# Kernel optimization log

Hardware: AMD Instinct MI355X
Metric: run time of the kernel (lower is better)

## Reference

```python
import jax, jax.numpy as jnp
import numpy as np

N = 30000  # nodes per type (drug and protein)


def graph_conv(x, s, d, W, b):
    # DGL GraphConv, norm='both': h = D_in^{-1/2} A (D_out^{-1/2} x) W + b
    ones = jnp.ones(s.shape, dtype=x.dtype)
    deg_out = jnp.maximum(jax.ops.segment_sum(ones, s, num_segments=N), 1.0)
    deg_in = jnp.maximum(jax.ops.segment_sum(ones, d, num_segments=N), 1.0)
    xh = (x * deg_out[:, None] ** -0.5) @ W          # transform first (in > out)
    agg = jax.ops.segment_sum(xh[s], d, num_segments=N)  # gather-scatter over edges
    return agg * deg_in[:, None] ** -0.5 + b


def rgcn_channel(xd, xp, src_c, dst_c, W1c, b1c, W2c, b2c):
    # relations: 0 drug->drug, 1 drug->protein, 2 protein->drug, 3 protein->protein
    hd = jax.nn.relu(graph_conv(xd, src_c[0], dst_c[0], W1c[0], b1c[0])
                     + graph_conv(xp, src_c[2], dst_c[2], W1c[2], b1c[2]))
    hp = jax.nn.relu(graph_conv(xd, src_c[1], dst_c[1], W1c[1], b1c[1])
                     + graph_conv(xp, src_c[3], dst_c[3], W1c[3], b1c[3]))
    hd2 = jax.nn.relu(graph_conv(hd, src_c[0], dst_c[0], W2c[0], b2c[0])
                      + graph_conv(hp, src_c[2], dst_c[2], W2c[2], b2c[2]))
    hp2 = jax.nn.relu(graph_conv(hd, src_c[1], dst_c[1], W2c[1], b2c[1])
                      + graph_conv(hp, src_c[3], dst_c[3], W2c[3], b2c[3]))
    return hd2, hp2


def semantic_attention(z, Wp, bp, q):
    # z: [N, K, F] -> beta [K], emb [N, F]
    w = jnp.tanh(z @ Wp + bp) @ q            # [N, K]
    beta = jax.nn.softmax(jnp.mean(w, axis=0))  # [K]
    return beta, jnp.einsum('k,nkf->nf', beta, z)


def setup_inputs() -> dict:
    key = jax.random.key(0)
    ks = jax.random.split(key, 8)
    E = 250000
    in_f, hid_f, out_f = 512, 256, 128
    x_drug = jax.random.normal(ks[0], (N, in_f), dtype=jnp.float32)
    x_pro = jax.random.normal(ks[1], (N, in_f), dtype=jnp.float32)
    src = jax.random.randint(ks[2], (4, 4, E), 0, N, dtype=jnp.int32)
    dst = jax.random.randint(ks[3], (4, 4, E), 0, N, dtype=jnp.int32)
    W1 = jax.random.normal(ks[4], (4, 4, in_f, hid_f), dtype=jnp.float32) / np.sqrt(in_f)
    b1 = jnp.zeros((4, 4, hid_f), dtype=jnp.float32)
    W2 = jax.random.normal(ks[5], (4, 4, hid_f, out_f), dtype=jnp.float32) / np.sqrt(hid_f)
    b2 = jnp.zeros((4, 4, out_f), dtype=jnp.float32)
    Wp = jax.random.normal(ks[6], (out_f, out_f), dtype=jnp.float32) / np.sqrt(out_f)
    bp = jnp.zeros((out_f,), dtype=jnp.float32)
    q = jax.random.normal(ks[7], (out_f,), dtype=jnp.float32) / np.sqrt(out_f)
    return {"x_drug": x_drug, "x_pro": x_pro, "src": src, "dst": dst,
            "W1": W1, "b1": b1, "W2": W2, "b2": b2, "Wp": Wp, "bp": bp, "q": q}


def reference(x_drug, x_pro, src, dst, W1, b1, W2, b2, Wp, bp, q):
    h_drug, h_pro = [], []
    for c in range(4):  # 4 channel graphs (fixed small loop)
        hd, hp = rgcn_channel(x_drug, x_pro, src[c], dst[c], W1[c], b1[c], W2[c], b2[c])
        h_drug.append(hd)
        h_pro.append(hp)
    # MCKRL stacks channels 0, 2, 3 only
    z_drug = jnp.stack([h_drug[0], h_drug[2], h_drug[3]], axis=1)  # [N,3,F]
    z_pro = jnp.stack([h_pro[0], h_pro[2], h_pro[3]], axis=1)
    beta_drug, emb_drug = semantic_attention(z_drug, Wp, bp, q)
    beta_pro, emb_pro = semantic_attention(z_pro, Wp, bp, q)
    return emb_drug, emb_pro, beta_drug, beta_pro
```

## Files before the change

### kernel.cpp

```cpp
#include <hip/hip_runtime.h>
#include <math.h>


#define IN_F  512
#define HID_F 256
#define OUT_F 128
#define NG    12
#define NPART 16
#define RANGE 1875
#define ES    8

typedef _Float16 f16x2 __attribute__((ext_vector_type(2)));
typedef _Float16 f16x4 __attribute__((ext_vector_type(4)));
typedef _Float16 f16x8 __attribute__((ext_vector_type(8)));
typedef float    f32x4 __attribute__((ext_vector_type(4)));

#define AS1 __attribute__((address_space(1)))
#define AS3 __attribute__((address_space(3)))

__device__ __forceinline__ void gld16(const void* g, void* l) {
    __builtin_amdgcn_global_load_lds((const AS1 void*)g, (AS3 void*)l, 16, 0, 0);
}

__host__ __device__ __forceinline__ int chan_of(int ci) { return ci == 0 ? 0 : ci + 1; }

__global__ __launch_bounds__(512) void k_hist(const int* __restrict__ src,
                                              const int* __restrict__ dst,
                                              int* __restrict__ hin,
                                              int* __restrict__ hout,
                                              int N, int E) {
    __shared__ int hi[RANGE], ho[RANGE];
    int g = blockIdx.x, p = blockIdx.y, es = blockIdx.z, t = threadIdx.x;
    for (int i = t; i < RANGE; i += 512) { hi[i] = 0; ho[i] = 0; }
    __syncthreads();
    int ci = g >> 2, c = chan_of(ci), r = g & 3;
    const int* sp = src + (size_t)(c * 4 + r) * E;
    const int* dp = dst + (size_t)(c * 4 + r) * E;
    int lo = p * RANGE;
    int sl = E / ES;
    int e0 = es * sl, e1 = (es == ES - 1) ? E : e0 + sl;
    for (int e = e0 + t; e < e1; e += 512) {
        int s = sp[e] - lo;
        int d = dp[e] - lo;
        if ((unsigned)s < (unsigned)RANGE) atomicAdd(&ho[s], 1);
        if ((unsigned)d < (unsigned)RANGE) atomicAdd(&hi[d], 1);
    }
    __syncthreads();
    int* hing  = hin  + ((size_t)g * ES + es) * N;
    int* houtg = hout + ((size_t)g * ES + es) * N;
    for (int i = t; i < RANGE; i += 512) {
        int node = lo + i;
        if (node < N) { hing[node] = hi[i]; houtg[node] = ho[i]; }
    }
}

__global__ void k_rs2(const int* __restrict__ hin, const int* __restrict__ hout,
                      int* __restrict__ deg_in,
                      float* __restrict__ rs_out, float* __restrict__ rs_in, int N) {
    int i = blockIdx.x * 256 + threadIdx.x;
    if (i >= NG * N) return;
    int g = i / N, n = i - g * N;
    int di = 0, dq = 0;
#pragma unroll
    for (int es = 0; es < ES; ++es) {
        di += hin [((size_t)g * ES + es) * N + n];
        dq += hout[((size_t)g * ES + es) * N + n];
    }
    deg_in[i] = di;
    rs_in[i]  = rsqrtf(fmaxf((float)di, 1.0f));
    rs_out[i] = rsqrtf(fmaxf((float)dq, 1.0f));
}

__global__ __launch_bounds__(1024) void k_scan(const int* __restrict__ deg_in,
                                               int* __restrict__ row_ptr, int N) {
    int g = blockIdx.x;
    const int* dg = deg_in + (size_t)g * N;
    int* rp = row_ptr + (size_t)g * (N + 1);
    __shared__ int wsum[16];
    int tid = threadIdx.x;
    int lane = tid & 63, wv = tid >> 6;
    int run = 0;
    for (int basei = 0; basei < N; basei += 1024) {
        int i = basei + tid;
        int v = (i < N) ? dg[i] : 0;
        int x = v;
#pragma unroll
        for (int off = 1; off < 64; off <<= 1) {
            int y = __shfl_up(x, off);
            if (lane >= off) x += y;
        }
        if (lane == 63) wsum[wv] = x;
        __syncthreads();
        if (wv == 0) {
            int s = (lane < 16) ? wsum[lane] : 0;
#pragma unroll
            for (int off = 1; off < 16; off <<= 1) {
                int y = __shfl_up(s, off);
                if (lane >= off) s += y;
            }
            if (lane < 16) wsum[lane] = s;
        }
        __syncthreads();
        int woff = wv ? wsum[wv - 1] : 0;
        if (i < N) rp[i] = run + woff + x - v;
        run += wsum[15];
        __syncthreads();
    }
    if (tid == 0) rp[N] = run;
}

__global__ __launch_bounds__(512) void k_fill3(const int* __restrict__ src,
                                               const int* __restrict__ dst,
                                               const int* __restrict__ row_ptr,
                                               const int* __restrict__ hin,
                                               int* __restrict__ col, int N, int E) {
    __shared__ int cur[RANGE];
    int g = blockIdx.x, p = blockIdx.y, es = blockIdx.z, t = threadIdx.x;
    int lo = p * RANGE;
    const int* rp = row_ptr + (size_t)g * (N + 1);
    for (int i = t; i < RANGE; i += 512) {
        int node = lo + i;
        int base = 0;
        if (node < N) {
            base = rp[node];
            for (int e2 = 0; e2 < es; ++e2)
                base += hin[((size_t)g * ES + e2) * N + node];
        }
        cur[i] = base;
    }
    __syncthreads();
    int ci = g >> 2, c = chan_of(ci), r = g & 3;
    const int* sp = src + (size_t)(c * 4 + r) * E;
    const int* dp = dst + (size_t)(c * 4 + r) * E;
    int* cg = col + (size_t)g * E;
    int sl = E / ES;
    int e0 = es * sl, e1 = (es == ES - 1) ? E : e0 + sl;
    for (int e = e0 + t; e < e1; e += 512) {
        int s = sp[e];
        int d = dp[e] - lo;
        if ((unsigned)d < (unsigned)RANGE) {
            int pos = atomicAdd(&cur[d], 1);
            cg[pos] = s;
        }
    }
}

__global__ void k_cvt16(const float* __restrict__ in, _Float16* __restrict__ out,
                        size_t n) {
    size_t i = ((size_t)blockIdx.x * 256 + threadIdx.x) * 8;
    if (i >= n) return;
    float4 a = *(const float4*)(in + i);
    float4 b = *(const float4*)(in + i + 4);
    f16x8 v;
    v[0] = (_Float16)a.x; v[1] = (_Float16)a.y; v[2] = (_Float16)a.z; v[3] = (_Float16)a.w;
    v[4] = (_Float16)b.x; v[5] = (_Float16)b.y; v[6] = (_Float16)b.z; v[7] = (_Float16)b.w;
    *(f16x8*)(out + i) = v;
}

__global__ __launch_bounds__(256) void k_cvtT(const float* __restrict__ W,
                                              _Float16* __restrict__ out,
                                              int K, int Nn) {
    __shared__ float tile[32][33];
    int gi = blockIdx.z, ci = gi >> 2, c = chan_of(ci), r = gi & 3;
    const float* Wg = W + (size_t)(c * 4 + r) * K * Nn;
    _Float16* Wo = out + ((size_t)(ci * 2 + (r >> 1)) * 2 * Nn + (size_t)(r & 1) * Nn) * K;
    int k0 = blockIdx.x * 32, n0 = blockIdx.y * 32;
    int tx = threadIdx.x & 31, ty = threadIdx.x >> 5;
    for (int yy = ty; yy < 32; yy += 8)
        tile[yy][tx] = Wg[(size_t)(k0 + yy) * Nn + n0 + tx];
    __syncthreads();
    for (int yy = ty; yy < 32; yy += 8)
        Wo[(size_t)(n0 + yy) * K + k0 + tx] = (_Float16)tile[tx][yy];
}

__global__ __launch_bounds__(256) void k_cvtWp(const float* __restrict__ Wp,
                                               _Float16* __restrict__ WpT) {
    __shared__ float tile[32][33];
    int k0 = blockIdx.x * 32, n0 = blockIdx.y * 32;
    int tx = threadIdx.x & 31, ty = threadIdx.x >> 5;
    for (int yy = ty; yy < 32; yy += 8)
        tile[yy][tx] = Wp[(size_t)(k0 + yy) * 128 + n0 + tx];
    __syncthreads();
    for (int yy = ty; yy < 32; yy += 8)
        WpT[(size_t)(n0 + yy) * 128 + k0 + tx] = (_Float16)tile[tx][yy];
}

__global__ __launch_bounds__(256) void k_gemm16(const _Float16* __restrict__ A0, size_t Azs,
                                                const _Float16* __restrict__ B0, size_t Bzs,
                                                _Float16* __restrict__ C0, size_t Czs,
                                                const float* __restrict__ rs0, int rsN,
                                                int Nsplit,
                                                int M, int K, int Nn) {
    const _Float16* A = A0 + (size_t)blockIdx.z * Azs;
    const _Float16* Bt = B0 + (size_t)blockIdx.z * Bzs;
    _Float16* C = C0 + (size_t)blockIdx.z * Czs;
    const float* rsA = rs0 ? rs0 + (size_t)(2 * blockIdx.z) * rsN : nullptr;
    __shared__ __align__(16) _Float16 As[128 * 64];
    __shared__ __align__(16) _Float16 Bs[128 * 64];
    int t = threadIdx.x;
    int lane = t & 63, wid = t >> 6;
    int wm = wid >> 1, wn = wid & 1;
    int brow = blockIdx.y * 128, bcol = blockIdx.x * 128;

    f32x4 acc[4][4] = {};
    int mrow = lane & 15;
    int khalf = lane >> 4;

    for (int k0 = 0; k0 < K; k0 += 64) {
        __syncthreads();
#pragma unroll
        for (int i = 0; i < 4; ++i) {
            int L = t + i * 256;
            int row = L >> 3, spp = L & 7;
            int sg = spp ^ (row & 7);
            int ra = brow + row; if (ra > M - 1) ra = M - 1;
            gld16((const void*)(A + (size_t)ra * K + (size_t)(k0 + sg * 8)),
                  (void*)(As + (size_t)(i * 256 + wid * 64) * 8));
            int rb = bcol + row;
            gld16((const void*)(Bt + (size_t)rb * K + (size_t)(k0 + sg * 8)),
                  (void*)(Bs + (size_t)(i * 256 + wid * 64) * 8));
        }
        __syncthreads();
#pragma unroll
        for (int ks = 0; ks < 2; ++ks) {
            f16x8 af[4], bf[4];
#pragma unroll
            for (int mi = 0; mi < 4; ++mi) {
                int r = wm * 64 + mi * 16 + mrow;
                int s = ks * 4 + khalf;
                int ph = s ^ (r & 7);
                af[mi] = *(const f16x8*)(As + r * 64 + ph * 8);
            }
#pragma unroll
            for (int ni = 0; ni < 4; ++ni) {
                int r = wn * 64 + ni * 16 + mrow;
                int s = ks * 4 + khalf;
                int ph = s ^ (r & 7);
                bf[ni] = *(const f16x8*)(Bs + r * 64 + ph * 8);
            }
#pragma unroll
            for (int mi = 0; mi < 4; ++mi)
#pragma unroll
                for (int ni = 0; ni < 4; ++ni)
                    acc[mi][ni] = __builtin_amdgcn_mfma_f32_16x16x32_f16(
                        af[mi], bf[ni], acc[mi][ni], 0, 0, 0);
        }
    }
#pragma unroll
    for (int mi = 0; mi < 4; ++mi) {
#pragma unroll
        for (int r = 0; r < 4; ++r) {
            int row = brow + wm * 64 + mi * 16 + (lane >> 4) * 4 + r;
            if (row < M) {
                float sA = 1.0f, sB = 1.0f;
                if (rsA) { sA = rsA[row]; sB = rsA[rsN + row]; }
#pragma unroll
                for (int ni = 0; ni < 4; ++ni) {
                    int colx = bcol + wn * 64 + ni * 16 + (lane & 15);
                    float sc = (colx < Nsplit) ? sA : sB;
                    C[(size_t)row * Nn + colx] = (_Float16)(acc[mi][ni][r] * sc);
                }
            }
        }
    }
}

template<typename FV, int VEC>
__device__ __forceinline__ void agg_body(const _Float16* __restrict__ Ya0,
                                         const _Float16* __restrict__ Yb0, int ystride,
                                         const int* __restrict__ row_ptr,
                                         const int* __restrict__ col,
                                         const float* __restrict__ rs_in,
                                         int ga0, int gb0,
                                         const float* __restrict__ ba0,
                                         const float* __restrict__ bb0,
                                         _Float16* __restrict__ outb,
                                         size_t out_sidestride, int ostride,
                                         int F, int N, int E) {
    int wv = threadIdx.x >> 6, lane = threadIdx.x & 63;
    int i = blockIdx.x * 4 + wv;
    if (i >= N) return;
    int side = blockIdx.y;
    int f0 = VEC * lane;
    const _Float16* Ya = Ya0 + side * F;
    const _Float16* Yb = Yb0 + side * F;
    int ga = ga0 + side, gb = gb0 + side;

    float accA[VEC] = {}, accB[VEC] = {};
    {
        const int* rp = row_ptr + (size_t)ga * (N + 1);
        const int* cg = col + (size_t)ga * E;
        int beg = rp[i], end = rp[i + 1];
        for (int e = beg; e < end; e += 4) {
            int s0 = cg[e];
            bool b1 = e + 1 < end, b2 = e + 2 < end, b3 = e + 3 < end;
            int s1 = b1 ? cg[e + 1] : s0;
            int s2 = b2 ? cg[e + 2] : s0;
            int s3 = b3 ? cg[e + 3] : s0;
            FV v0 = *(const FV*)(Ya + (size_t)s0 * ystride + f0);
            FV v1 = *(const FV*)(Ya + (size_t)s1 * ystride + f0);
            FV v2 = *(const FV*)(Ya + (size_t)s2 * ystride + f0);
            FV v3 = *(const FV*)(Ya + (size_t)s3 * ystride + f0);
            float m1 = b1 ? 1.0f : 0.0f, m2 = b2 ? 1.0f : 0.0f, m3 = b3 ? 1.0f : 0.0f;
#pragma unroll
            for (int k = 0; k < VEC; ++k)
                accA[k] += (float)v0[k] + m1 * (float)v1[k]
                         + m2 * (float)v2[k] + m3 * (float)v3[k];
        }
    }
    {
        const int* rp = row_ptr + (size_t)gb * (N + 1);
        const int* cg = col + (size_t)gb * E;
        int beg = rp[i], end = rp[i + 1];
        for (int e = beg; e < end; e += 4) {
            int s0 = cg[e];
            bool b1 = e + 1 < end, b2 = e + 2 < end, b3 = e + 3 < end;
            int s1 = b1 ? cg[e + 1] : s0;
            int s2 = b2 ? cg[e + 2] : s0;
            int s3 = b3 ? cg[e + 3] : s0;
            FV v0 = *(const FV*)(Yb + (size_t)s0 * ystride + f0);
            FV v1 = *(const FV*)(Yb + (size_t)s1 * ystride + f0);
            FV v2 = *(const FV*)(Yb + (size_t)s2 * ystride + f0);
            FV v3 = *(const FV*)(Yb + (size_t)s3 * ystride + f0);
            float m1 = b1 ? 1.0f : 0.0f, m2 = b2 ? 1.0f : 0.0f, m3 = b3 ? 1.0f : 0.0f;
#pragma unroll
            for (int k = 0; k < VEC; ++k)
                accB[k] += (float)v0[k] + m1 * (float)v1[k]
                         + m2 * (float)v2[k] + m3 * (float)v3[k];
        }
    }
    float ria = rs_in[(size_t)ga * N + i];
    float rib = rs_in[(size_t)gb * N + i];
    FV o;
#pragma unroll
    for (int k = 0; k < VEC; ++k) {
        float v = ria * accA[k] + rib * accB[k]
                + ba0[side * F + f0 + k] + bb0[side * F + f0 + k];
        o[k] = (_Float16)fmaxf(v, 0.0f);
    }
    *(FV*)(outb + side * out_sidestride + (size_t)i * ostride + f0) = o;
}

__global__ __launch_bounds__(256) void k_agg256(const _Float16* Ya0, const _Float16* Yb0,
                                                int ystride, const int* row_ptr, const int* col,
                                                const float* rs_in, int ga0, int gb0,
                                                const float* ba0, const float* bb0,
                                                _Float16* outb, size_t oss, int ostride,
                                                int N, int E) {
    agg_body<f16x4, 4>(Ya0, Yb0, ystride, row_ptr, col, rs_in, ga0, gb0,
                       ba0, bb0, outb, oss, ostride, 256, N, E);
}

__global__ __launch_bounds__(256) void k_agg128(const _Float16* Ya0, const _Float16* Yb0,
                                                int ystride, const int* row_ptr, const int* col,
                                                const float* rs_in, int ga0, int gb0,
                                                const float* ba0, const float* bb0,
                                                _Float16* outb, size_t oss, int ostride,
                                                int N, int E) {
    agg_body<f16x2, 2>(Ya0, Yb0, ystride, row_ptr, col, rs_in, ga0, gb0,
                       ba0, bb0, outb, oss, ostride, 128, N, E);
}

__global__ __launch_bounds__(256) void k_wred(const _Float16* __restrict__ T,
                                              const float* __restrict__ bp,
                                              const float* __restrict__ q,
                                              float* __restrict__ w_all, int N) {
    int m = blockIdx.x * 4 + (threadIdx.x >> 6);
    int lane = threadIdx.x & 63;
    if (m >= 6 * N) return;
    f16x2 v2 = *(const f16x2*)(T + (size_t)m * 128 + 2 * lane);
    float v = tanhf((float)v2[0] + bp[2 * lane]) * q[2 * lane]
            + tanhf((float)v2[1] + bp[2 * lane + 1]) * q[2 * lane + 1];
#pragma unroll
    for (int o = 1; o < 64; o <<= 1) v += __shfl_xor(v, o);
    if (lane == 0) {
        int side = m / (3 * N);
        int rem = m - side * 3 * N;
        int node = rem / 3, k = rem - node * 3;
        w_all[((size_t)side * 3 + k) * N + node] = v;
    }
}

__global__ __launch_bounds__(256) void k_beta(const float* __restrict__ w_all,
                                              float* __restrict__ beta_ws,
                                              float* __restrict__ beta_out, int N) {
    int side = blockIdx.x;
    int tid = threadIdx.x;
    __shared__ float red[256];
    float sums[3];
    for (int k = 0; k < 3; ++k) {
        float s = 0.0f;
        for (int i = tid; i < N; i += 256) s += w_all[((size_t)side * 3 + k) * N + i];
        red[tid] = s;
        __syncthreads();
        for (int off = 128; off > 0; off >>= 1) {
            if (tid < off) red[tid] += red[tid + off];
            __syncthreads();
        }
        sums[k] = red[0];
        __syncthreads();
    }
    if (tid == 0) {
        float inv = 1.0f / (float)N;
        float m0 = sums[0] * inv, m1 = sums[1] * inv, m2 = sums[2] * inv;
        float mx = fmaxf(m0, fmaxf(m1, m2));
        float e0 = expf(m0 - mx), e1 = expf(m1 - mx), e2 = expf(m2 - mx);
        float denom = e0 + e1 + e2;
        float b0 = e0 / denom, b1 = e1 / denom, b2 = e2 / denom;
        beta_ws[side * 3 + 0] = b0; beta_out[side * 3 + 0] = b0;
        beta_ws[side * 3 + 1] = b1; beta_out[side * 3 + 1] = b1;
        beta_ws[side * 3 + 2] = b2; beta_out[side * 3 + 2] = b2;
    }
}

__global__ __launch_bounds__(64) void k_emb(const _Float16* __restrict__ z,
                                            const float* __restrict__ beta_ws,
                                            float* __restrict__ out, int N) {
    int i = blockIdx.x, side = blockIdx.y, t = threadIdx.x;
    const _Float16* zr = z + (size_t)side * N * 384 + (size_t)i * 384;
    const float* b = beta_ws + side * 3;
    f16x2 z0 = *(const f16x2*)(zr + 2 * t);
    f16x2 z1 = *(const f16x2*)(zr + 128 + 2 * t);
    f16x2 z2 = *(const f16x2*)(zr + 256 + 2 * t);
    float2 o;
    o.x = b[0] * (float)z0[0] + b[1] * (float)z1[0] + b[2] * (float)z2[0];
    o.y = b[0] * (float)z0[1] + b[1] * (float)z1[1] + b[2] * (float)z2[1];
    *(float2*)&out[(size_t)side * N * 128 + (size_t)i * 128 + 2 * t] = o;
}

extern "C" void kernel_launch(void* const* d_in, const int* in_sizes, int n_in,
                              void* d_out, int out_size, void* d_ws, size_t ws_size,
                              hipStream_t stream) {
    const float* x_drug = (const float*)d_in[0];
    const float* x_pro  = (const float*)d_in[1];
    const int*   src    = (const int*)d_in[2];
    const int*   dst    = (const int*)d_in[3];
    const float* W1     = (const float*)d_in[4];
    const float* b1     = (const float*)d_in[5];
    const float* W2     = (const float*)d_in[6];
    const float* b2     = (const float*)d_in[7];
    const float* Wp     = (const float*)d_in[8];
    const float* bp     = (const float*)d_in[9];
    const float* q      = (const float*)d_in[10];
    float* out = (float*)d_out;

    const int N = in_sizes[0] / IN_F;
    const int E = in_sizes[2] / 16;

    size_t off = 0;
    auto alloc = [&](size_t bytes) -> void* {
        void* p = (char*)d_ws + off;
        off += (bytes + 255) & ~(size_t)255;
        return p;
    };
    int*      deg_in  = (int*)alloc((size_t)NG * N * 4);
    int*      row_ptr = (int*)alloc((size_t)NG * (N + 1) * 4);
    int*      col     = (int*)alloc((size_t)NG * E * 4);
    float*    rs_out  = (float*)alloc((size_t)NG * N * 4);
    float*    rs_in   = (float*)alloc((size_t)NG * N * 4);
    _Float16* xh      = (_Float16*)alloc((size_t)2 * N * IN_F * 2);
    _Float16* W1cat   = (_Float16*)alloc((size_t)6 * 2 * HID_F * IN_F * 2);
    _Float16* W2cat   = (_Float16*)alloc((size_t)6 * 2 * OUT_F * HID_F * 2);
    _Float16* WpT     = (_Float16*)alloc((size_t)128 * 128 * 2);
    _Float16* Y1      = (_Float16*)alloc((size_t)2 * N * 512 * 2);
    _Float16* Y2      = (_Float16*)alloc((size_t)2 * N * 256 * 2);
    _Float16* H1      = (_Float16*)alloc((size_t)2 * N * HID_F * 2);
    _Float16* zbuf    = (_Float16*)alloc((size_t)2 * N * 384 * 2);
    float*    w_all   = (float*)alloc((size_t)2 * 3 * N * 4);
    float*    beta_ws = (float*)alloc(64);
    int*      hin  = (int*)Y1;
    int*      hout = hin + (size_t)NG * ES * N;
    _Float16* T    = Y1;
    (void)ws_size; (void)n_in; (void)out_size;

    dim3 hg(NG, NPART, ES);
    k_hist<<<hg, 512, 0, stream>>>(src, dst, hin, hout, N, E);
    k_rs2<<<(NG * N + 255) / 256, 256, 0, stream>>>(hin, hout, deg_in, rs_out, rs_in, N);
    k_scan<<<NG, 1024, 0, stream>>>(deg_in, row_ptr, N);
    k_fill3<<<hg, 512, 0, stream>>>(src, dst, row_ptr, hin, col, N, E);

    size_t nx = (size_t)N * IN_F;
    k_cvt16<<<(int)((nx / 8 + 255) / 256), 256, 0, stream>>>(x_drug, xh, nx);
    k_cvt16<<<(int)((nx / 8 + 255) / 256), 256, 0, stream>>>(x_pro,  xh + nx, nx);
    k_cvtT<<<dim3(IN_F / 32, HID_F / 32, NG), 256, 0, stream>>>(W1, W1cat, IN_F, HID_F);
    k_cvtT<<<dim3(HID_F / 32, OUT_F / 32, NG), 256, 0, stream>>>(W2, W2cat, HID_F, OUT_F);
    k_cvtWp<<<dim3(4, 4), 256, 0, stream>>>(Wp, WpT);

    dim3 g1(512 / 128, (N + 127) / 128, 2);
    dim3 g2(256 / 128, (N + 127) / 128, 2);
    dim3 agrid((N + 3) / 4, 2);
    dim3 egrid(N, 2);

    for (int ci = 0; ci < 3; ++ci) {
        int c = chan_of(ci);
        k_gemm16<<<g1, 256, 0, stream>>>(xh, (size_t)N * IN_F,
                                         W1cat + (size_t)ci * 2 * 512 * 512, (size_t)512 * 512,
                                         Y1, (size_t)N * 512,
                                         rs_out + (size_t)ci * 4 * N, N, 256,
                                         N, IN_F, 512);
        k_agg256<<<agrid, 256, 0, stream>>>(Y1, Y1 + (size_t)N * 512, 512,
                                            row_ptr, col, rs_in,
                                            ci * 4 + 0, ci * 4 + 2,
                                            b1 + (size_t)c * 4 * HID_F, b1 + (size_t)(c * 4 + 2) * HID_F,
                                            H1, (size_t)N * HID_F, HID_F, N, E);
        k_gemm16<<<g2, 256, 0, stream>>>(H1, (size_t)N * HID_F,
                                         W2cat + (size_t)ci * 2 * 256 * 256, (size_t)256 * 256,
                                         Y2, (size_t)N * 256,
                                         rs_out + (size_t)ci * 4 * N, N, 128,
                                         N, HID_F, 256);
        k_agg128<<<agrid, 256, 0, stream>>>(Y2, Y2 + (size_t)N * 256, 256,
                                            row_ptr, col, rs_in,
                                            ci * 4 + 0, ci * 4 + 2,
                                            b2 + (size_t)c * 4 * OUT_F, b2 + (size_t)(c * 4 + 2) * OUT_F,
                                            zbuf + (size_t)ci * OUT_F, (size_t)N * 384, 384, N, E);
    }

    int Mrows = 2 * N * 3;
    dim3 gT(1, (Mrows + 127) / 128, 1);
    k_gemm16<<<gT, 256, 0, stream>>>(zbuf, 0, WpT, 0, T, 0,
                                     nullptr, 0, 0, Mrows, 128, 128);
    k_wred<<<(Mrows + 3) / 4, 256, 0, stream>>>(T, bp, q, w_all, N);
    k_beta<<<2, 256, 0, stream>>>(w_all, beta_ws, out + (size_t)2 * N * OUT_F, N);
    k_emb<<<egrid, 64, 0, stream>>>(zbuf, beta_ws, out, N);
}
```

Measured before the change: 1.216 ms.

## Unroll aggregation gather by 8, parallelize beta reduction, batch emb and convert launches

The aggregation kernel's two relation loops become one unrolled loop that gathers eight neighbor rows per iteration instead of four, which raises memory-level parallelism for the irregular gathers. The semantic-attention beta reduction is split into a wide partial-sum kernel and a small finalize kernel, replacing the two-block serial reduction. The embedding kernel now packs four rows per 256-thread block instead of one row per 64-thread block. The two fp16 input conversions are merged into one launch. The wider unroll raises register pressure and adds masked work on short adjacency lists.

```diff
diff --git a/kernel.cpp b/kernel.cpp
--- a/kernel.cpp
+++ b/kernel.cpp
@@ -9,6 +9,7 @@
 #define NPART 16
 #define RANGE 1875
 #define ES    8
+#define BCH   32
 
 typedef _Float16 f16x2 __attribute__((ext_vector_type(2)));
 typedef _Float16 f16x4 __attribute__((ext_vector_type(4)));
@@ -145,16 +146,17 @@
     }
 }
 
-__global__ void k_cvt16(const float* __restrict__ in, _Float16* __restrict__ out,
-                        size_t n) {
+__global__ void k_cvt16b(const float* __restrict__ inA, const float* __restrict__ inB,
+                         _Float16* __restrict__ out, size_t n) {
     size_t i = ((size_t)blockIdx.x * 256 + threadIdx.x) * 8;
     if (i >= n) return;
+    const float* in = blockIdx.y ? inB : inA;
     float4 a = *(const float4*)(in + i);
     float4 b = *(const float4*)(in + i + 4);
     f16x8 v;
     v[0] = (_Float16)a.x; v[1] = (_Float16)a.y; v[2] = (_Float16)a.z; v[3] = (_Float16)a.w;
     v[4] = (_Float16)b.x; v[5] = (_Float16)b.y; v[6] = (_Float16)b.z; v[7] = (_Float16)b.w;
-    *(f16x8*)(out + i) = v;
+    *(f16x8*)(out + blockIdx.y * n + i) = v;
 }
 
 __global__ __launch_bounds__(256) void k_cvtT(const float* __restrict__ W,
@@ -282,59 +284,41 @@
     if (i >= N) return;
     int side = blockIdx.y;
     int f0 = VEC * lane;
-    const _Float16* Ya = Ya0 + side * F;
-    const _Float16* Yb = Yb0 + side * F;
-    int ga = ga0 + side, gb = gb0 + side;
-
-    float accA[VEC] = {}, accB[VEC] = {};
-    {
-        const int* rp = row_ptr + (size_t)ga * (N + 1);
-        const int* cg = col + (size_t)ga * E;
+    const _Float16* Ybase[2] = { Ya0 + side * F, Yb0 + side * F };
+    int gg[2] = { ga0 + side, gb0 + side };
+
+    float accT[2][VEC] = {};
+#pragma unroll
+    for (int h = 0; h < 2; ++h) {
+        const int* rp = row_ptr + (size_t)gg[h] * (N + 1);
+        const int* cg = col + (size_t)gg[h] * E;
+        const _Float16* Y = Ybase[h];
         int beg = rp[i], end = rp[i + 1];
-        for (int e = beg; e < end; e += 4) {
-            int s0 = cg[e];
-            bool b1 = e + 1 < end, b2 = e + 2 < end, b3 = e + 3 < end;
-            int s1 = b1 ? cg[e + 1] : s0;
-            int s2 = b2 ? cg[e + 2] : s0;
-            int s3 = b3 ? cg[e + 3] : s0;
-            FV v0 = *(const FV*)(Ya + (size_t)s0 * ystride + f0);
-            FV v1 = *(const FV*)(Ya + (size_t)s1 * ystride + f0);
-            FV v2 = *(const FV*)(Ya + (size_t)s2 * ystride + f0);
-            FV v3 = *(const FV*)(Ya + (size_t)s3 * ystride + f0);
-            float m1 = b1 ? 1.0f : 0.0f, m2 = b2 ? 1.0f : 0.0f, m3 = b3 ? 1.0f : 0.0f;
-#pragma unroll
-            for (int k = 0; k < VEC; ++k)
-                accA[k] += (float)v0[k] + m1 * (float)v1[k]
-                         + m2 * (float)v2[k] + m3 * (float)v3[k];
-        }
-    }
-    {
-        const int* rp = row_ptr + (size_t)gb * (N + 1);
-        const int* cg = col + (size_t)gb * E;
-        int beg = rp[i], end = rp[i + 1];
-        for (int e = beg; e < end; e += 4) {
-            int s0 = cg[e];
-            bool b1 = e + 1 < end, b2 = e + 2 < end, b3 = e + 3 < end;
-            int s1 = b1 ? cg[e + 1] : s0;
-            int s2 = b2 ? cg[e + 2] : s0;
-            int s3 = b3 ? cg[e + 3] : s0;
-            FV v0 = *(const FV*)(Yb + (size_t)s0 * ystride + f0);
-            FV v1 = *(const FV*)(Yb + (size_t)s1 * ystride + f0);
-            FV v2 = *(const FV*)(Yb + (size_t)s2 * ystride + f0);
-            FV v3 = *(const FV*)(Yb + (size_t)s3 * ystride + f0);
-            float m1 = b1 ? 1.0f : 0.0f, m2 = b2 ? 1.0f : 0.0f, m3 = b3 ? 1.0f : 0.0f;
-#pragma unroll
-            for (int k = 0; k < VEC; ++k)
-                accB[k] += (float)v0[k] + m1 * (float)v1[k]
-                         + m2 * (float)v2[k] + m3 * (float)v3[k];
-        }
-    }
-    float ria = rs_in[(size_t)ga * N + i];
-    float rib = rs_in[(size_t)gb * N + i];
+        for (int e = beg; e < end; e += 8) {
+            int idx[8]; float m[8]; FV v[8];
+            idx[0] = cg[e]; m[0] = 1.0f;
+#pragma unroll
+            for (int u = 1; u < 8; ++u) {
+                bool ok = (e + u < end);
+                idx[u] = ok ? cg[e + u] : idx[0];
+                m[u] = ok ? 1.0f : 0.0f;
+            }
+#pragma unroll
+            for (int u = 0; u < 8; ++u)
+                v[u] = *(const FV*)(Y + (size_t)idx[u] * ystride + f0);
+#pragma unroll
+            for (int u = 0; u < 8; ++u)
+#pragma unroll
+                for (int k = 0; k < VEC; ++k)
+                    accT[h][k] = fmaf(m[u], (float)v[u][k], accT[h][k]);
+        }
+    }
+    float ria = rs_in[(size_t)gg[0] * N + i];
+    float rib = rs_in[(size_t)gg[1] * N + i];
     FV o;
 #pragma unroll
     for (int k = 0; k < VEC; ++k) {
-        float v = ria * accA[k] + rib * accB[k]
+        float v = ria * accT[0][k] + rib * accT[1][k]
                 + ba0[side * F + f0 + k] + bb0[side * F + f0 + k];
         o[k] = (_Float16)fmaxf(v, 0.0f);
     }
@@ -381,28 +365,43 @@
     }
 }
 
-__global__ __launch_bounds__(256) void k_beta(const float* __restrict__ w_all,
+__global__ __launch_bounds__(256) void k_beta1(const float* __restrict__ w_all,
+                                               float* __restrict__ partials, int N) {
+    int chunk = blockIdx.x, k = blockIdx.y, side = blockIdx.z;
+    const float* w = w_all + ((size_t)side * 3 + k) * N;
+    int per = (N + BCH - 1) / BCH;
+    int i0 = chunk * per;
+    int i1 = i0 + per; if (i1 > N) i1 = N;
+    int tid = threadIdx.x;
+    float s = 0.0f;
+    for (int i = i0 + tid; i < i1; i += 256) s += w[i];
+    __shared__ float red[256];
+    red[tid] = s;
+    __syncthreads();
+    for (int off = 128; off > 0; off >>= 1) {
+        if (tid < off) red[tid] += red[tid + off];
+        __syncthreads();
+    }
+    if (tid == 0) partials[((size_t)side * 3 + k) * BCH + chunk] = red[0];
+}
+
+__global__ __launch_bounds__(64) void k_beta2(const float* __restrict__ partials,
                                               float* __restrict__ beta_ws,
                                               float* __restrict__ beta_out, int N) {
-    int side = blockIdx.x;
+    __shared__ float sums[6];
     int tid = threadIdx.x;
-    __shared__ float red[256];
-    float sums[3];
-    for (int k = 0; k < 3; ++k) {
+    if (tid < 6) {
         float s = 0.0f;
-        for (int i = tid; i < N; i += 256) s += w_all[((size_t)side * 3 + k) * N + i];
-        red[tid] = s;
-        __syncthreads();
-        for (int off = 128; off > 0; off >>= 1) {
-            if (tid < off) red[tid] += red[tid + off];
-            __syncthreads();
-        }
-        sums[k] = red[0];
-        __syncthreads();
-    }
-    if (tid == 0) {
+        for (int j = 0; j < BCH; ++j) s += partials[(size_t)tid * BCH + j];
+        sums[tid] = s;
+    }
+    __syncthreads();
+    if (tid < 2) {
+        int side = tid;
         float inv = 1.0f / (float)N;
-        float m0 = sums[0] * inv, m1 = sums[1] * inv, m2 = sums[2] * inv;
+        float m0 = sums[side * 3 + 0] * inv;
+        float m1 = sums[side * 3 + 1] * inv;
+        float m2 = sums[side * 3 + 2] * inv;
         float mx = fmaxf(m0, fmaxf(m1, m2));
         float e0 = expf(m0 - mx), e1 = expf(m1 - mx), e2 = expf(m2 - mx);
         float denom = e0 + e1 + e2;
@@ -413,10 +412,12 @@
     }
 }
 
-__global__ __launch_bounds__(64) void k_emb(const _Float16* __restrict__ z,
-                                            const float* __restrict__ beta_ws,
-                                            float* __restrict__ out, int N) {
-    int i = blockIdx.x, side = blockIdx.y, t = threadIdx.x;
+__global__ __launch_bounds__(256) void k_emb(const _Float16* __restrict__ z,
+                                             const float* __restrict__ beta_ws,
+                                             float* __restrict__ out, int N) {
+    int i = blockIdx.x * 4 + (threadIdx.x >> 6);
+    if (i >= N) return;
+    int side = blockIdx.y, t = threadIdx.x & 63;
     const _Float16* zr = z + (size_t)side * N * 384 + (size_t)i * 384;
     const float* b = beta_ws + side * 3;
     f16x2 z0 = *(const f16x2*)(zr + 2 * t);
@@ -467,6 +468,7 @@
     _Float16* H1      = (_Float16*)alloc((size_t)2 * N * HID_F * 2);
     _Float16* zbuf    = (_Float16*)alloc((size_t)2 * N * 384 * 2);
     float*    w_all   = (float*)alloc((size_t)2 * 3 * N * 4);
+    float*    partials= (float*)alloc((size_t)6 * BCH * 4);
     float*    beta_ws = (float*)alloc(64);
     int*      hin  = (int*)Y1;
     int*      hout = hin + (size_t)NG * ES * N;
@@ -480,8 +482,7 @@
     k_fill3<<<hg, 512, 0, stream>>>(src, dst, row_ptr, hin, col, N, E);
 
     size_t nx = (size_t)N * IN_F;
-    k_cvt16<<<(int)((nx / 8 + 255) / 256), 256, 0, stream>>>(x_drug, xh, nx);
-    k_cvt16<<<(int)((nx / 8 + 255) / 256), 256, 0, stream>>>(x_pro,  xh + nx, nx);
+    k_cvt16b<<<dim3((int)((nx / 8 + 255) / 256), 2), 256, 0, stream>>>(x_drug, x_pro, xh, nx);
     k_cvtT<<<dim3(IN_F / 32, HID_F / 32, NG), 256, 0, stream>>>(W1, W1cat, IN_F, HID_F);
     k_cvtT<<<dim3(HID_F / 32, OUT_F / 32, NG), 256, 0, stream>>>(W2, W2cat, HID_F, OUT_F);
     k_cvtWp<<<dim3(4, 4), 256, 0, stream>>>(Wp, WpT);
@@ -489,7 +490,6 @@
     dim3 g1(512 / 128, (N + 127) / 128, 2);
     dim3 g2(256 / 128, (N + 127) / 128, 2);
     dim3 agrid((N + 3) / 4, 2);
-    dim3 egrid(N, 2);
 
     for (int ci = 0; ci < 3; ++ci) {
         int c = chan_of(ci);
@@ -520,6 +520,7 @@
     k_gemm16<<<gT, 256, 0, stream>>>(zbuf, 0, WpT, 0, T, 0,
                                      nullptr, 0, 0, Mrows, 128, 128);
     k_wred<<<(Mrows + 3) / 4, 256, 0, stream>>>(T, bp, q, w_all, N);
-    k_beta<<<2, 256, 0, stream>>>(w_all, beta_ws, out + (size_t)2 * N * OUT_F, N);
-    k_emb<<<egrid, 64, 0, stream>>>(zbuf, beta_ws, out, N);
-}
+    k_beta1<<<dim3(BCH, 3, 2), 256, 0, stream>>>(w_all, partials, N);
+    k_beta2<<<1, 64, 0, stream>>>(partials, beta_ws, out + (size_t)2 * N * OUT_F, N);
+    k_emb<<<agrid, 256, 0, stream>>>(zbuf, beta_ws, out, N);
+}
```

Result: faster. 1.116 ms (-8.2%).
